# Performance work log

Hardware: AMD Instinct MI355X
Metric: run time of the kernel (lower is better)

## Reference

```python
import jax, jax.numpy as jnp
import numpy as np

V = 10000   # vocab size
H = 768     # HIDDEN_SIZE
B = 8       # batch
S = 512     # padded seq len
L = 8       # TRANSFORMER_LAYERS
EPS = 1e-5  # torch LayerNorm default eps


def setup_inputs() -> dict:
    key = jax.random.key(0)
    ks = jax.random.split(key, 16)
    init = lambda k, shape: jax.random.normal(k, shape, jnp.float32) * 0.02
    x = jax.random.randint(ks[0], (B, S), 0, V)
    # full-length sequences: avoids NaN from the original's softmax(dim=1) over
    # fully -inf padded columns (same behavior as torch for this input)
    lengths = jnp.full((B,), S, dtype=jnp.int32)
    return {
        'x': x,
        'lengths': lengths,
        'emb_w': init(ks[1], (V, H)),
        'Wq': init(ks[2], (L, H, H)), 'bq': jnp.zeros((L, H), jnp.float32),
        'Wk': init(ks[3], (L, H, H)), 'bk': jnp.zeros((L, H), jnp.float32),
        'Wv': init(ks[4], (L, H, H)), 'bv': jnp.zeros((L, H), jnp.float32),
        'W1': init(ks[5], (L, H, H)), 'b1': jnp.zeros((L, H), jnp.float32),
        'W2': init(ks[6], (L, H, H)), 'b2': jnp.zeros((L, H), jnp.float32),
        'g1': jnp.ones((L, H), jnp.float32), 'be1': jnp.zeros((L, H), jnp.float32),
        'g2': jnp.ones((L, H), jnp.float32), 'be2': jnp.zeros((L, H), jnp.float32),
        'fc_w': init(ks[7], (H, H)), 'fc_b': jnp.zeros((H,), jnp.float32),
    }


def _layernorm(x, g, b):
    m = jnp.mean(x, axis=-1, keepdims=True)
    v = jnp.mean(jnp.square(x - m), axis=-1, keepdims=True)
    return (x - m) * jax.lax.rsqrt(v + EPS) * g + b


def _pos_encoding(seq, dim):
    pos = jnp.arange(seq, dtype=jnp.float32)[:, None]
    div = jnp.exp(jnp.arange(0, dim, 2, dtype=jnp.float32) * (-np.log(10000.0) / dim))
    ang = pos * div[None, :]                                  # [S, H/2]
    return jnp.stack([jnp.sin(ang), jnp.cos(ang)], axis=-1).reshape(seq, dim)


def reference(x, lengths, emb_w, Wq, bq, Wk, bk, Wv, bv, W1, b1, W2, b2,
              g1, be1, g2, be2, fc_w, fc_b):
    z = emb_w[x] + _pos_encoding(S, H)[None]                  # [B,S,H]
    causal = jnp.tril(jnp.ones((S, S), bool))                 # [S,S]
    valid = jnp.arange(S)[None, :] < lengths[:, None]         # [B,S]
    mask = causal[None] & valid[:, None, :] & valid[:, :, None]  # [B,S,S]
    scale = 1.0 / jnp.sqrt(jnp.float32(H))
    for i in range(L):
        q = z @ Wq[i] + bq[i]
        k = z @ Wk[i] + bk[i]
        v = z @ Wv[i] + bv[i]
        scores = jnp.einsum('bqh,bkh->bqk', q, k) * scale
        scores = jnp.where(mask, scores, -jnp.inf)
        # NOTE: original code applies softmax over dim=1 (query axis) — faithful
        atten = jax.nn.softmax(scores, axis=1)
        out = jnp.einsum('bqk,bkh->bqh', atten, v)
        o1 = _layernorm(z + out, g1[i], be1[i])               # eval: dropout=identity
        mid = jax.nn.relu(o1 @ W1[i] + b1[i]) @ W2[i] + b2[i]
        z = _layernorm(mid + o1, g2[i], be2[i])
    zf = z @ fc_w + fc_b                                      # [B,S,H]
    logits = jnp.einsum('bsh,vh->bsv', zf, emb_w)             # [B,S,V]
    return jax.nn.softmax(logits, axis=-1)
```

## Files before the change

### kernel.cpp

```cpp
#include <hip/hip_runtime.h>
#include <math.h>

typedef unsigned int   u32;
typedef unsigned short u16;
typedef __attribute__((ext_vector_type(8))) short bf16x8;
typedef __attribute__((ext_vector_type(4))) float f32x4;
typedef __attribute__((ext_vector_type(4))) unsigned short u16x4;
typedef __attribute__((ext_vector_type(8))) unsigned short u16x8;

#define HID   768
#define SEQ   512
#define BATCH 8
#define LAYERS 8
#define VOC   10000
#define NROWS (BATCH*SEQ)
#define NH    ((long long)NROWS*HID)
#define SS8   ((long long)BATCH*SEQ*SEQ)
#define EPSLN 1e-5f
#define WSZ   ((long long)HID*HID)

__device__ __forceinline__ u16 f2bf(float f) {
    u32 u = __builtin_bit_cast(u32, f);
    return (u16)((u + 0x7fffu + ((u >> 16) & 1u)) >> 16);
}
__device__ __forceinline__ float bf2f(u16 h) {
    return __builtin_bit_cast(float, (u32)h << 16);
}

__device__ __forceinline__ void async16(u16* lds, const u16* g) {
    __builtin_amdgcn_global_load_lds(
        (const __attribute__((address_space(1))) u32*)g,
        (__attribute__((address_space(3))) u32*)lds, 16, 0, 0);
}

__global__ __launch_bounds__(256) void embed_kernel(
    const int* __restrict__ x, const float* __restrict__ emb,
    float* __restrict__ Z, u16* __restrict__ Zh)
{
    const int row = blockIdx.x;
    const int s   = row & (SEQ - 1);
    const int tok = x[row];
    const long long base  = (long long)row * HID;
    const long long ebase = (long long)tok * HID;
    const float coef = -0.0239852613853544f;
    #pragma unroll
    for (int j = 0; j < 3; ++j) {
        const int h = threadIdx.x + 256 * j;
        const int i = h >> 1;
        const float ang = (float)s * expf((float)i * coef);
        const float pe  = (h & 1) ? cosf(ang) : sinf(ang);
        const float v = emb[ebase + h] + pe;
        Z[base + h]  = v;
        Zh[base + h] = f2bf(v);
    }
}

__global__ __launch_bounds__(256) void convert_emb(
    const float* __restrict__ e, u16* __restrict__ eh)
{
    const long long i = ((long long)blockIdx.x * 256 + threadIdx.x) * 4;
    const float4 v = *(const float4*)&e[i];
    u16x4 p;
    p[0] = f2bf(v.x); p[1] = f2bf(v.y); p[2] = f2bf(v.z); p[3] = f2bf(v.w);
    *(u16x4*)&eh[i] = p;
}

__global__ __launch_bounds__(256) void transp_all(
    const float* __restrict__ Wq, const float* __restrict__ Wk,
    const float* __restrict__ Wv, const float* __restrict__ W1,
    const float* __restrict__ W2, const float* __restrict__ fcw,
    u16* __restrict__ WT)
{
    __shared__ u16 tile[32][34];
    const int z = blockIdx.z;
    const float* src;
    long long doff;
    if (z < 40) {
        const int lyr = z / 5, idx = z % 5;
        const float* bases[5] = {Wq, Wk, Wv, W1, W2};
        src  = bases[idx] + (long long)lyr * WSZ;
        doff = ((long long)lyr * 5 + idx) * WSZ;
    } else {
        src = fcw; doff = 40LL * WSZ;
    }
    u16* D = WT + doff;
    const int n0 = blockIdx.x * 32, k0 = blockIdx.y * 32;
    const int c = threadIdx.x & 31, r0 = threadIdx.x >> 5;
    #pragma unroll
    for (int p = 0; p < 4; ++p)
        tile[r0 + 8*p][c] = f2bf(src[(long long)(k0 + r0 + 8*p) * HID + n0 + c]);
    __syncthreads();
    #pragma unroll
    for (int p = 0; p < 4; ++p)
        D[(long long)(n0 + r0 + 8*p) * HID + k0 + c] = tile[c][r0 + 8*p];
}

__global__ void pack_bias_all(const float* __restrict__ bq,
                              const float* __restrict__ bk,
                              const float* __restrict__ bv,
                              float* __restrict__ dst)
{
    const int part = blockIdx.x, l = blockIdx.y, h = threadIdx.x;
    const float* src = part == 0 ? bq : (part == 1 ? bk : bv);
    dst[((long long)l*3 + part) * HID + h] = src[(long long)l*HID + h];
}

template<bool RELU, bool OUT_BF16, bool XISM, bool VSPLIT>
__global__ __launch_bounds__(256) void gemm_mfma(
    const u16* __restrict__ A, int lda, long long sA,
    const u16* __restrict__ B, int ldb, long long sB,
    void* __restrict__ Cp, int ldc, long long sC,
    int N, int K, const float* __restrict__ bias, float alpha,
    u16* __restrict__ vt)
{
    __shared__ u16 As[2][128 * 32];
    __shared__ u16 Bs[2][128 * 32];
    const int bz = blockIdx.z;
    const int m0 = (XISM ? blockIdx.x : blockIdx.y) * 128;
    const int n0 = (XISM ? blockIdx.y : blockIdx.x) * 128;
    const int t = threadIdx.x, w = t >> 6, l = t & 63;
    const int lrow = l >> 2, lk8 = (l & 3) * 8;
    const int wm = (w >> 1) * 64, wn = (w & 1) * 64;
    A += sA * bz; B += sB * bz;

    f32x4 acc[4][4];
    #pragma unroll
    for (int mi = 0; mi < 4; ++mi)
        #pragma unroll
        for (int ni = 0; ni < 4; ++ni) acc[mi][ni] = (f32x4){0.f,0.f,0.f,0.f};

    auto stage = [&](int buf, int k0) {
        #pragma unroll
        for (int r = 0; r < 2; ++r) {
            const int seg = w * 2 + r;
            async16(&As[buf][seg * 512],
                    A + (long long)(m0 + seg*16 + lrow) * lda + (k0 + lk8));
        }
        #pragma unroll
        for (int r = 0; r < 2; ++r) {
            const int seg = w * 2 + r;
            int row = n0 + seg*16 + lrow;
            row = row < N ? row : N - 1;
            async16(&Bs[buf][seg * 512], B + (long long)row * ldb + (k0 + lk8));
        }
    };
    const int fr = l & 15, fk = (l >> 4) * 8;
    auto compute = [&](int cur) {
        bf16x8 af[4], bfr[4];
        #pragma unroll
        for (int mi = 0; mi < 4; ++mi)
            af[mi] = *(const bf16x8*)&As[cur][(wm + mi*16 + fr) * 32 + fk];
        #pragma unroll
        for (int ni = 0; ni < 4; ++ni)
            bfr[ni] = *(const bf16x8*)&Bs[cur][(wn + ni*16 + fr) * 32 + fk];
        #pragma unroll
        for (int mi = 0; mi < 4; ++mi)
            #pragma unroll
            for (int ni = 0; ni < 4; ++ni)
                acc[mi][ni] = __builtin_amdgcn_mfma_f32_16x16x32_bf16(
                    af[mi], bfr[ni], acc[mi][ni], 0, 0, 0);
    };

    const int NS = K >> 5;
    stage(0, 0);
    for (int tt = 0; tt < NS; ++tt) {
        if (tt + 1 < NS) {
            stage((tt + 1) & 1, (tt + 1) << 5);
            asm volatile("s_waitcnt vmcnt(4)\n\ts_barrier" ::: "memory");
        } else {
            asm volatile("s_waitcnt vmcnt(0)\n\ts_barrier" ::: "memory");
        }
        compute(tt & 1);
        asm volatile("s_barrier" ::: "memory");
    }

    float* Cf = (float*)Cp + sC * bz;
    u16*   Ch = (u16*)Cp + sC * bz;
    const int fq = l >> 4;
    #pragma unroll
    for (int ni = 0; ni < 4; ++ni) {
        const int col = n0 + wn + ni*16 + fr;
        const bool ok = col < N;
        const float bv = (bias && ok) ? bias[col] : 0.f;
        #pragma unroll
        for (int mi = 0; mi < 4; ++mi) {
            const int row0 = m0 + wm + mi*16 + fq*4;
            if constexpr (VSPLIT) {
                if (col < 1536) {
                    #pragma unroll
                    for (int v = 0; v < 4; ++v)
                        Ch[(long long)(row0 + v) * ldc + col] =
                            f2bf(alpha * acc[mi][ni][v] + bv);
                } else {
                    const int b9 = row0 >> 9, s9 = row0 & 511;
                    u16x4 pk;
                    #pragma unroll
                    for (int v = 0; v < 4; ++v)
                        pk[v] = f2bf(alpha * acc[mi][ni][v] + bv);
                    *(u16x4*)&vt[((long long)b9 * HID + (col - 1536)) * SEQ + s9] = pk;
                }
            } else {
                #pragma unroll
                for (int v = 0; v < 4; ++v) {
                    float val = alpha * acc[mi][ni][v] + bv;
                    if (RELU) val = fmaxf(val, 0.f);
                    if (ok) {
                        if (OUT_BF16) Ch[(long long)(row0 + v) * ldc + col] = f2bf(val);
                        else          Cf[(long long)(row0 + v) * ldc + col] = val;
                    }
                }
            }
        }
    }
}

template<bool RELU, bool OUT_BF16>
__global__ __launch_bounds__(128) void gemm_small(
    const u16* __restrict__ A, int lda, long long sA,
    const u16* __restrict__ B, int ldb, long long sB,
    void* __restrict__ Cp, int ldc, long long sC,
    int N, int K, const float* __restrict__ bias, float alpha)
{
    __shared__ u16 As[2][64 * 64];
    __shared__ u16 Bs[2][64 * 64];
    const int bz = blockIdx.z;
    const int n0 = blockIdx.x * 64;
    const int m0 = blockIdx.y * 64;
    const int t = threadIdx.x, w = t >> 6, l = t & 63;
    const int srow = l >> 3;
    const int skof = ((l & 7) ^ srow) * 8;
    const int wm = w * 32;
    A += sA * bz; B += sB * bz;

    f32x4 acc[2][4];
    #pragma unroll
    for (int mi = 0; mi < 2; ++mi)
        #pragma unroll
        for (int ni = 0; ni < 4; ++ni) acc[mi][ni] = (f32x4){0.f,0.f,0.f,0.f};

    auto stage = [&](int buf, int k0) {
        #pragma unroll
        for (int r = 0; r < 4; ++r) {
            const int seg = w * 4 + r;
            const int row = seg * 8 + srow;
            async16(&As[buf][seg * 512],
                    A + (long long)(m0 + row) * lda + (k0 + skof));
        }
        #pragma unroll
        for (int r = 0; r < 4; ++r) {
            const int seg = w * 4 + r;
            const int row = seg * 8 + srow;
            async16(&Bs[buf][seg * 512],
                    B + (long long)(n0 + row) * ldb + (k0 + skof));
        }
    };
    const int fr = l & 15, fkb = l >> 4;
    auto compute = [&](int cur) {
        #pragma unroll
        for (int ks = 0; ks < 2; ++ks) {
            const int ps = ((ks * 4 + fkb) ^ (fr & 7)) * 8;
            bf16x8 af[2], bfv[4];
            #pragma unroll
            for (int mi = 0; mi < 2; ++mi)
                af[mi] = *(const bf16x8*)&As[cur][(wm + mi*16 + fr) * 64 + ps];
            #pragma unroll
            for (int ni = 0; ni < 4; ++ni)
                bfv[ni] = *(const bf16x8*)&Bs[cur][(ni*16 + fr) * 64 + ps];
            #pragma unroll
            for (int mi = 0; mi < 2; ++mi)
                #pragma unroll
                for (int ni = 0; ni < 4; ++ni)
                    acc[mi][ni] = __builtin_amdgcn_mfma_f32_16x16x32_bf16(
                        af[mi], bfv[ni], acc[mi][ni], 0, 0, 0);
        }
    };

    const int NS = K >> 6;
    stage(0, 0);
    for (int tt = 0; tt < NS; ++tt) {
        if (tt + 1 < NS) {
            stage((tt + 1) & 1, (tt + 1) << 6);
            asm volatile("s_waitcnt vmcnt(8)\n\ts_barrier" ::: "memory");
        } else {
            asm volatile("s_waitcnt vmcnt(0)\n\ts_barrier" ::: "memory");
        }
        compute(tt & 1);
        asm volatile("s_barrier" ::: "memory");
    }

    float* Cf = (float*)Cp + sC * bz;
    u16*   Ch = (u16*)Cp + sC * bz;
    const int fq = l >> 4;
    #pragma unroll
    for (int ni = 0; ni < 4; ++ni) {
        const int col = n0 + ni*16 + fr;
        const float bv = bias ? bias[col] : 0.f;
        #pragma unroll
        for (int mi = 0; mi < 2; ++mi) {
            const int row0 = m0 + wm + mi*16 + fq*4;
            #pragma unroll
            for (int v = 0; v < 4; ++v) {
                float val = alpha * acc[mi][ni][v] + bv;
                if (RELU) val = fmaxf(val, 0.f);
                if (OUT_BF16) Ch[(long long)(row0 + v) * ldc + col] = f2bf(val);
                else          Cf[(long long)(row0 + v) * ldc + col] = val;
            }
        }
    }
}

__global__ __launch_bounds__(256) void gemm_conv(
    const u16* __restrict__ A, const float* __restrict__ Bf,
    u16* __restrict__ C)
{
    __shared__ u16 As[128 * 32];
    __shared__ u16 Bs[128 * 32];
    const int m0 = blockIdx.x * 128;
    const int n0 = blockIdx.y * 128;
    const int t = threadIdx.x, w = t >> 6, l = t & 63;
    const int lrow = l >> 2, lk8 = (l & 3) * 8;
    const int wm = (w >> 1) * 64, wn = (w & 1) * 64;
    f32x4 acc[4][4];
    #pragma unroll
    for (int mi = 0; mi < 4; ++mi)
        #pragma unroll
        for (int ni = 0; ni < 4; ++ni) acc[mi][ni] = (f32x4){0.f,0.f,0.f,0.f};

    for (int k0 = 0; k0 < HID; k0 += 32) {
        #pragma unroll
        for (int r = 0; r < 2; ++r) {
            const int seg = w * 2 + r;
            async16(&As[seg * 512],
                    A + (long long)(m0 + seg*16 + lrow) * HID + (k0 + lk8));
        }
        #pragma unroll
        for (int r = 0; r < 2; ++r) {
            const int flat = r * 2048 + t * 8;
            int row = n0 + (flat >> 5);
            row = row < VOC ? row : VOC - 1;
            const float* g = Bf + (long long)row * HID + (k0 + (flat & 31));
            const float4 v0 = *(const float4*)g;
            const float4 v1 = *(const float4*)(g + 4);
            bf16x8 hv;
            hv[0]=(short)f2bf(v0.x); hv[1]=(short)f2bf(v0.y);
            hv[2]=(short)f2bf(v0.z); hv[3]=(short)f2bf(v0.w);
            hv[4]=(short)f2bf(v1.x); hv[5]=(short)f2bf(v1.y);
            hv[6]=(short)f2bf(v1.z); hv[7]=(short)f2bf(v1.w);
            *(bf16x8*)&Bs[flat] = hv;
        }
        __syncthreads();
        const int fr = l & 15, fk = (l >> 4) * 8;
        bf16x8 af[4], bfr[4];
        #pragma unroll
        for (int mi = 0; mi < 4; ++mi)
            af[mi] = *(const bf16x8*)&As[(wm + mi*16 + fr) * 32 + fk];
        #pragma unroll
        for (int ni = 0; ni < 4; ++ni)
            bfr[ni] = *(const bf16x8*)&Bs[(wn + ni*16 + fr) * 32 + fk];
        #pragma unroll
        for (int mi = 0; mi < 4; ++mi)
            #pragma unroll
            for (int ni = 0; ni < 4; ++ni)
                acc[mi][ni] = __builtin_amdgcn_mfma_f32_16x16x32_bf16(
                    af[mi], bfr[ni], acc[mi][ni], 0, 0, 0);
        __syncthreads();
    }
    const int fr = l & 15, fq = l >> 4;
    #pragma unroll
    for (int ni = 0; ni < 4; ++ni) {
        const int col = n0 + wn + ni*16 + fr;
        if (col >= VOC) continue;
        #pragma unroll
        for (int mi = 0; mi < 4; ++mi) {
            const int row0 = m0 + wm + mi*16 + fq*4;
            #pragma unroll
            for (int v = 0; v < 4; ++v)
                C[(long long)(row0 + v) * (2*VOC) + col] = f2bf(acc[mi][ni][v]);
        }
    }
}

__global__ __launch_bounds__(256) void softmax_q_kernel(
    const float* __restrict__ sc, u16* __restrict__ att,
    const int* __restrict__ lengths)
{
    const int b  = blockIdx.x;
    const int k0 = blockIdx.y * 16;
    const int tx = threadIdx.x & 15;
    const int ty = threadIdx.x >> 4;
    const int c  = k0 + tx;
    const int len = lengths[b];
    const float* base  = sc  + (long long)b * SEQ * SEQ;
    u16*         obase = att + (long long)b * SEQ * SEQ;
    const bool cvalid = (c < len);

    float vals[32];
    float m = -3.0e38f, ssum = 0.f;
    #pragma unroll
    for (int i = 0; i < 32; ++i) {
        const int q = ty + 16 * i;
        float xv = -3.0e38f;
        if (cvalid && c <= q && q < len)
            xv = base[(long long)q * SEQ + c];
        vals[i] = xv;
        if (xv > m) { ssum = ssum * __expf(m - xv) + 1.f; m = xv; }
        else if (xv > -3.0e38f) { ssum += __expf(xv - m); }
    }
    __shared__ float ms[16][17], ss[16][17];
    ms[ty][tx] = m; ss[ty][tx] = ssum;
    __syncthreads();
    if (ty == 0) {
        float M = ms[0][tx];
        #pragma unroll
        for (int r = 1; r < 16; ++r) M = fmaxf(M, ms[r][tx]);
        float Sx = 0.f;
        #pragma unroll
        for (int r = 0; r < 16; ++r) Sx += ss[r][tx] * __expf(ms[r][tx] - M);
        ms[0][tx] = M; ss[0][tx] = Sx;
    }
    __syncthreads();
    const float M   = ms[0][tx];
    const float den = ss[0][tx];
    const float inv = (den > 0.f) ? 1.f / den : 0.f;
    #pragma unroll
    for (int i = 0; i < 32; ++i) {
        const int q = ty + 16 * i;
        obase[(long long)q * SEQ + c] = f2bf(__expf(vals[i] - M) * inv);
    }
}

__global__ __launch_bounds__(256) void ln_add_kernel(
    const float* __restrict__ Xa, const float* __restrict__ Xb,
    float* __restrict__ O, u16* __restrict__ Oh,
    const float* __restrict__ g, const float* __restrict__ be)
{
    const int row = blockIdx.x;
    const long long base = (long long)row * HID;
    const int t = threadIdx.x;
    const float x0 = Xa[base + t]       + Xb[base + t];
    const float x1 = Xa[base + t + 256] + Xb[base + t + 256];
    const float x2 = Xa[base + t + 512] + Xb[base + t + 512];
    __shared__ float r1[4], r2[4];
    float s = x0 + x1 + x2;
    #pragma unroll
    for (int o = 32; o; o >>= 1) s += __shfl_down(s, o, 64);
    if ((t & 63) == 0) r1[t >> 6] = s;
    __syncthreads();
    const float mean = (r1[0] + r1[1] + r1[2] + r1[3]) * (1.f / HID);
    const float d0 = x0 - mean, d1 = x1 - mean, d2 = x2 - mean;
    float v = d0*d0 + d1*d1 + d2*d2;
    #pragma unroll
    for (int o = 32; o; o >>= 1) v += __shfl_down(v, o, 64);
    if ((t & 63) == 0) r2[t >> 6] = v;
    __syncthreads();
    const float var = (r2[0] + r2[1] + r2[2] + r2[3]) * (1.f / HID);
    const float rs = rsqrtf(var + EPSLN);
    const float y0 = d0 * rs * g[t]       + be[t];
    const float y1 = d1 * rs * g[t + 256] + be[t + 256];
    const float y2 = d2 * rs * g[t + 512] + be[t + 512];
    O[base + t]        = y0;  Oh[base + t]       = f2bf(y0);
    O[base + t + 256]  = y1;  Oh[base + t + 256] = f2bf(y1);
    O[base + t + 512]  = y2;  Oh[base + t + 512] = f2bf(y2);
}

__global__ __launch_bounds__(256) void softmax_v_kernel(float* __restrict__ out)
{
    __shared__ float row[VOC];
    __shared__ float rm[4], rs_[4];
    const long long obase = (long long)blockIdx.x * VOC;
    const u16* lg = (const u16*)out + 2 * obase + VOC;
    const int t = threadIdx.x;
    float m = -3.0e38f, s = 0.f;
    for (int i = t * 8; i < VOC; i += 2048) {
        const u16x8 h8 = *(const u16x8*)&lg[i];
        #pragma unroll
        for (int j = 0; j < 8; ++j) {
            const float xv = bf2f(h8[j]);
            row[i + j] = xv;
            const float d = xv - m;
            if (d > 0.f) { s = s * __expf(-d) + 1.f; m = xv; }
            else         { s += __expf(d); }
        }
    }
    #pragma unroll
    for (int o = 32; o; o >>= 1) {
        const float om = __shfl_down(m, o, 64), os = __shfl_down(s, o, 64);
        const float M = fmaxf(m, om);
        s = s * __expf(m - M) + os * __expf(om - M);
        m = M;
    }
    if ((t & 63) == 0) { rm[t >> 6] = m; rs_[t >> 6] = s; }
    __syncthreads();
    const float M = fmaxf(fmaxf(rm[0], rm[1]), fmaxf(rm[2], rm[3]));
    const float S = rs_[0]*__expf(rm[0]-M) + rs_[1]*__expf(rm[1]-M)
                  + rs_[2]*__expf(rm[2]-M) + rs_[3]*__expf(rm[3]-M);
    const float inv = 1.f / S;
    for (int i = t * 4; i < VOC; i += 1024) {
        float4 v = *(const float4*)&row[i];
        v.x = __expf(v.x - M) * inv;
        v.y = __expf(v.y - M) * inv;
        v.z = __expf(v.z - M) * inv;
        v.w = __expf(v.w - M) * inv;
        *(float4*)&out[obase + i] = v;
    }
}

extern "C" void kernel_launch(void* const* d_in, const int* in_sizes, int n_in,
                              void* d_out, int out_size, void* d_ws, size_t ws_size,
                              hipStream_t stream)
{
    const int*   x    = (const int*)  d_in[0];
    const int*   lens = (const int*)  d_in[1];
    const float* emb  = (const float*)d_in[2];
    const float* Wq   = (const float*)d_in[3];
    const float* bq   = (const float*)d_in[4];
    const float* Wk   = (const float*)d_in[5];
    const float* bk   = (const float*)d_in[6];
    const float* Wv   = (const float*)d_in[7];
    const float* bv   = (const float*)d_in[8];
    const float* W1   = (const float*)d_in[9];
    const float* b1   = (const float*)d_in[10];
    const float* W2   = (const float*)d_in[11];
    const float* b2   = (const float*)d_in[12];
    const float* g1   = (const float*)d_in[13];
    const float* be1  = (const float*)d_in[14];
    const float* g2   = (const float*)d_in[15];
    const float* be2  = (const float*)d_in[16];
    const float* fcw  = (const float*)d_in[17];
    const float* fcb  = (const float*)d_in[18];

    float* out = (float*)d_out;
    float* Zb     = out;
    float* O1f    = Zb + NH;
    float* M2f    = O1f + NH;
    float* SCORES = M2f + NH;
    float* BQKV   = SCORES + SS8;
    u16* ub   = (u16*)(BQKV + (long long)LAYERS * 2304);
    u16* Zbh  = ub;  ub += NH;
    u16* QKVh = ub;  ub += (long long)NROWS * 1536;
    u16* ATTB = ub;  ub += SS8;
    u16* Vt   = ub;  ub += NH;
    u16* O1h  = ub;  ub += NH;
    u16* M1h  = ub;  ub += NH;
    u16* WT   = ub;  ub += 41LL * WSZ;

    u16* ZFh = (u16*)d_ws;
    u16* EH  = ZFh + NH;
    const bool ehpath = ws_size >= (size_t)((NH + (long long)VOC * HID) * 2);
    u16* LOGH = (u16*)out + VOC;

    const float scale = 1.0f / sqrtf((float)HID);
    const dim3 blk(256), blk128(128);

    embed_kernel<<<NROWS, blk, 0, stream>>>(x, emb, Zb, Zbh);
    transp_all<<<dim3(24, 24, 41), blk, 0, stream>>>(Wq, Wk, Wv, W1, W2, fcw, WT);
    pack_bias_all<<<dim3(3, LAYERS), dim3(768), 0, stream>>>(bq, bk, bv, BQKV);
    if (ehpath) convert_emb<<<7500, blk, 0, stream>>>(emb, EH);

    for (int l = 0; l < LAYERS; ++l) {
        const u16* wl = WT + (long long)l * 5 * WSZ;

        gemm_mfma<false, true, false, true><<<dim3(18, 32), blk, 0, stream>>>(
            Zbh, HID, 0, wl, HID, 0, QKVh, 1536, 0,
            2304, HID, BQKV + (long long)l * 2304, 1.0f, Vt);

        gemm_small<false, false><<<dim3(8, 8, BATCH), blk128, 0, stream>>>(
            QKVh, 1536, (long long)SEQ * 1536,
            QKVh + 768, 1536, (long long)SEQ * 1536,
            SCORES, SEQ, (long long)SEQ * SEQ,
            512, HID, nullptr, scale);

        softmax_q_kernel<<<dim3(BATCH, SEQ/16), blk, 0, stream>>>(SCORES, ATTB, lens);

        gemm_small<false, false><<<dim3(12, 8, BATCH), blk128, 0, stream>>>(
            ATTB, SEQ, (long long)SEQ * SEQ,
            Vt, SEQ, (long long)HID * SEQ,
            O1f, HID, (long long)SEQ * HID,
            768, SEQ, nullptr, 1.0f);

        ln_add_kernel<<<NROWS, blk, 0, stream>>>(Zb, O1f, O1f, O1h,
                                                 g1 + l*HID, be1 + l*HID);
        gemm_small<true, true><<<dim3(12, 64), blk128, 0, stream>>>(
            O1h, HID, 0, wl + 3*WSZ, HID, 0, M1h, HID, 0,
            768, HID, b1 + l*HID, 1.0f);
        gemm_small<false, false><<<dim3(12, 64), blk128, 0, stream>>>(
            M1h, HID, 0, wl + 4*WSZ, HID, 0, M2f, HID, 0,
            768, HID, b2 + l*HID, 1.0f);
        ln_add_kernel<<<NROWS, blk, 0, stream>>>(M2f, O1f, Zb, Zbh,
                                                 g2 + l*HID, be2 + l*HID);
    }

    gemm_small<false, true><<<dim3(12, 64), blk128, 0, stream>>>(
        Zbh, HID, 0, WT + 40LL*WSZ, HID, 0, ZFh, HID, 0,
        768, HID, fcb, 1.0f);

    if (ehpath) {
        gemm_mfma<false, true, true, false><<<dim3(32, 79), blk, 0, stream>>>(
            ZFh, HID, 0, EH, HID, 0, LOGH, 2*VOC, 0,
            VOC, HID, nullptr, 1.0f, nullptr);
    } else {
        gemm_conv<<<dim3(32, 79), blk, 0, stream>>>(ZFh, emb, LOGH);
    }

    softmax_v_kernel<<<NROWS, blk, 0, stream>>>(out);
}
```

Measured before the change: 1.095 ms.

## Replace 128x128 MFMA GEMM with 256x256 swizzled 8-wave kernel; warp-per-row LayerNorm

The 128x128 MFMA GEMM used for the QKV projection and the vocab logits is replaced by a 512-thread kernel with 256x256 tiles, K-steps of 64 split into two halves, and an XOR-swizzled LDS layout. Global loads are interleaved between MFMA groups, with s_setprio raising wave priority around the matrix math. The intent is more reuse per tile, fewer LDS bank conflicts and better overlap of loads with compute. LayerNorm now handles one row per wavefront with float4 loads and shuffle-only reductions, removing shared-memory barriers. The larger tiles mean fewer blocks (144 for QKV) on a 256-CU part and higher register pressure, which may hurt occupancy.

```diff
diff --git a/kernel.cpp b/kernel.cpp
--- a/kernel.cpp
+++ b/kernel.cpp
@@ -105,110 +105,125 @@
     dst[((long long)l*3 + part) * HID + h] = src[(long long)l*HID + h];
 }
 
-template<bool RELU, bool OUT_BF16, bool XISM, bool VSPLIT>
-__global__ __launch_bounds__(256) void gemm_mfma(
-    const u16* __restrict__ A, int lda, long long sA,
-    const u16* __restrict__ B, int ldb, long long sB,
-    void* __restrict__ Cp, int ldc, long long sC,
-    int N, int K, const float* __restrict__ bias, float alpha,
-    u16* __restrict__ vt)
-{
-    __shared__ u16 As[2][128 * 32];
-    __shared__ u16 Bs[2][128 * 32];
-    const int bz = blockIdx.z;
-    const int m0 = (XISM ? blockIdx.x : blockIdx.y) * 128;
-    const int n0 = (XISM ? blockIdx.y : blockIdx.x) * 128;
+template<bool VSPLIT>
+__global__ __launch_bounds__(512) void gemm_8ph(
+    const u16* __restrict__ A, const u16* __restrict__ B,
+    u16* __restrict__ Cp, int ldc, int N, int K,
+    const float* __restrict__ bias, u16* __restrict__ vt)
+{
+    __shared__ u16 Ab[2][2][8192];
+    __shared__ u16 Bb[2][2][8192];
+    const int m0 = blockIdx.x * 256;
+    const int n0 = blockIdx.y * 256;
     const int t = threadIdx.x, w = t >> 6, l = t & 63;
-    const int lrow = l >> 2, lk8 = (l & 3) * 8;
-    const int wm = (w >> 1) * 64, wn = (w & 1) * 64;
-    A += sA * bz; B += sB * bz;
-
-    f32x4 acc[4][4];
-    #pragma unroll
-    for (int mi = 0; mi < 4; ++mi)
-        #pragma unroll
-        for (int ni = 0; ni < 4; ++ni) acc[mi][ni] = (f32x4){0.f,0.f,0.f,0.f};
-
-    auto stage = [&](int buf, int k0) {
+    const int fr = l & 15, jl = l >> 4;
+    const int wm = (w >> 2) * 128, wn = (w & 3) * 64;
+
+    f32x4 acc[8][4];
+    #pragma unroll
+    for (int mf = 0; mf < 8; ++mf)
+        #pragma unroll
+        for (int nf = 0; nf < 4; ++nf) acc[mf][nf] = (f32x4){0.f,0.f,0.f,0.f};
+
+    auto stageA = [&](int d, int h, int kt) {
         #pragma unroll
         for (int r = 0; r < 2; ++r) {
-            const int seg = w * 2 + r;
-            async16(&As[buf][seg * 512],
-                    A + (long long)(m0 + seg*16 + lrow) * lda + (k0 + lk8));
-        }
+            const int f16 = r * 512 + t;
+            const int row = f16 >> 2, j = f16 & 3;
+            const int kofs = kt + h * 32 + ((j ^ ((row >> 1) & 3)) << 3);
+            async16(&Ab[d][h][f16 * 8], A + (long long)(m0 + row) * K + kofs);
+        }
+    };
+    auto stageB = [&](int d, int h, int kt) {
         #pragma unroll
         for (int r = 0; r < 2; ++r) {
-            const int seg = w * 2 + r;
-            int row = n0 + seg*16 + lrow;
-            row = row < N ? row : N - 1;
-            async16(&Bs[buf][seg * 512], B + (long long)row * ldb + (k0 + lk8));
+            const int f16 = r * 512 + t;
+            const int row = f16 >> 2, j = f16 & 3;
+            int gr = n0 + row; gr = gr < N ? gr : N - 1;
+            const int kofs = kt + h * 32 + ((j ^ ((row >> 1) & 3)) << 3);
+            async16(&Bb[d][h][f16 * 8], B + (long long)gr * K + kofs);
         }
     };
-    const int fr = l & 15, fk = (l >> 4) * 8;
-    auto compute = [&](int cur) {
-        bf16x8 af[4], bfr[4];
-        #pragma unroll
-        for (int mi = 0; mi < 4; ++mi)
-            af[mi] = *(const bf16x8*)&As[cur][(wm + mi*16 + fr) * 32 + fk];
-        #pragma unroll
-        for (int ni = 0; ni < 4; ++ni)
-            bfr[ni] = *(const bf16x8*)&Bs[cur][(wn + ni*16 + fr) * 32 + fk];
-        #pragma unroll
-        for (int mi = 0; mi < 4; ++mi)
-            #pragma unroll
-            for (int ni = 0; ni < 4; ++ni)
-                acc[mi][ni] = __builtin_amdgcn_mfma_f32_16x16x32_bf16(
-                    af[mi], bfr[ni], acc[mi][ni], 0, 0, 0);
-    };
-
-    const int NS = K >> 5;
-    stage(0, 0);
-    for (int tt = 0; tt < NS; ++tt) {
-        if (tt + 1 < NS) {
-            stage((tt + 1) & 1, (tt + 1) << 5);
-            asm volatile("s_waitcnt vmcnt(4)\n\ts_barrier" ::: "memory");
-        } else {
-            asm volatile("s_waitcnt vmcnt(0)\n\ts_barrier" ::: "memory");
-        }
-        compute(tt & 1);
-        asm volatile("s_barrier" ::: "memory");
-    }
-
-    float* Cf = (float*)Cp + sC * bz;
-    u16*   Ch = (u16*)Cp + sC * bz;
-    const int fq = l >> 4;
-    #pragma unroll
-    for (int ni = 0; ni < 4; ++ni) {
-        const int col = n0 + wn + ni*16 + fr;
-        const bool ok = col < N;
-        const float bv = (bias && ok) ? bias[col] : 0.f;
-        #pragma unroll
-        for (int mi = 0; mi < 4; ++mi) {
-            const int row0 = m0 + wm + mi*16 + fq*4;
+
+    stageA(0, 0, 0); stageB(0, 0, 0); stageA(0, 1, 0); stageB(0, 1, 0);
+
+    const int NT = K >> 6;
+    for (int tt = 0; tt < NT; ++tt) {
+        const int d = tt & 1, kt1 = (tt + 1) << 6;
+        const bool more = (tt + 1) < NT;
+        #pragma unroll
+        for (int h = 0; h < 2; ++h) {
+            if (h == 0 || more) asm volatile("s_waitcnt vmcnt(4)" ::: "memory");
+            else                asm volatile("s_waitcnt vmcnt(0)" ::: "memory");
+            __builtin_amdgcn_s_barrier();
+            asm volatile("" ::: "memory");
+            if (more) stageA(d ^ 1, h, kt1);
+            bf16x8 bfr[4], af[4];
+            #pragma unroll
+            for (int nf = 0; nf < 4; ++nf) {
+                const int row = wn + nf * 16 + fr;
+                bfr[nf] = *(const bf16x8*)
+                    &Bb[d][h][row * 32 + ((jl ^ ((row >> 1) & 3)) << 3)];
+            }
+            #pragma unroll
+            for (int mi = 0; mi < 4; ++mi) {
+                const int row = wm + mi * 16 + fr;
+                af[mi] = *(const bf16x8*)
+                    &Ab[d][h][row * 32 + ((jl ^ ((row >> 1) & 3)) << 3)];
+            }
+            __builtin_amdgcn_s_setprio(1);
+            #pragma unroll
+            for (int mi = 0; mi < 4; ++mi)
+                #pragma unroll
+                for (int nf = 0; nf < 4; ++nf)
+                    acc[mi][nf] = __builtin_amdgcn_mfma_f32_16x16x32_bf16(
+                        af[mi], bfr[nf], acc[mi][nf], 0, 0, 0);
+            __builtin_amdgcn_s_setprio(0);
+            if (more) stageB(d ^ 1, h, kt1);
+            #pragma unroll
+            for (int mi = 0; mi < 4; ++mi) {
+                const int row = wm + (mi + 4) * 16 + fr;
+                af[mi] = *(const bf16x8*)
+                    &Ab[d][h][row * 32 + ((jl ^ ((row >> 1) & 3)) << 3)];
+            }
+            __builtin_amdgcn_s_setprio(1);
+            #pragma unroll
+            for (int mi = 0; mi < 4; ++mi)
+                #pragma unroll
+                for (int nf = 0; nf < 4; ++nf)
+                    acc[mi + 4][nf] = __builtin_amdgcn_mfma_f32_16x16x32_bf16(
+                        af[mi], bfr[nf], acc[mi + 4][nf], 0, 0, 0);
+            __builtin_amdgcn_s_setprio(0);
+        }
+    }
+
+    #pragma unroll
+    for (int nf = 0; nf < 4; ++nf) {
+        const int col = n0 + wn + nf * 16 + fr;
+        if (col >= N) continue;
+        const float bv = bias ? bias[col] : 0.f;
+        #pragma unroll
+        for (int mf = 0; mf < 8; ++mf) {
+            const int row0 = m0 + wm + mf * 16 + jl * 4;
             if constexpr (VSPLIT) {
                 if (col < 1536) {
                     #pragma unroll
                     for (int v = 0; v < 4; ++v)
-                        Ch[(long long)(row0 + v) * ldc + col] =
-                            f2bf(alpha * acc[mi][ni][v] + bv);
+                        Cp[(long long)(row0 + v) * ldc + col] =
+                            f2bf(acc[mf][nf][v] + bv);
                 } else {
                     const int b9 = row0 >> 9, s9 = row0 & 511;
                     u16x4 pk;
                     #pragma unroll
                     for (int v = 0; v < 4; ++v)
-                        pk[v] = f2bf(alpha * acc[mi][ni][v] + bv);
+                        pk[v] = f2bf(acc[mf][nf][v] + bv);
                     *(u16x4*)&vt[((long long)b9 * HID + (col - 1536)) * SEQ + s9] = pk;
                 }
             } else {
                 #pragma unroll
-                for (int v = 0; v < 4; ++v) {
-                    float val = alpha * acc[mi][ni][v] + bv;
-                    if (RELU) val = fmaxf(val, 0.f);
-                    if (ok) {
-                        if (OUT_BF16) Ch[(long long)(row0 + v) * ldc + col] = f2bf(val);
-                        else          Cf[(long long)(row0 + v) * ldc + col] = val;
-                    }
-                }
+                for (int v = 0; v < 4; ++v)
+                    Cp[(long long)(row0 + v) * ldc + col] =
+                        f2bf(acc[mf][nf][v] + bv);
             }
         }
     }
@@ -434,33 +449,45 @@
     float* __restrict__ O, u16* __restrict__ Oh,
     const float* __restrict__ g, const float* __restrict__ be)
 {
-    const int row = blockIdx.x;
+    const int row = blockIdx.x * 4 + (threadIdx.x >> 6);
+    const int l = threadIdx.x & 63;
     const long long base = (long long)row * HID;
-    const int t = threadIdx.x;
-    const float x0 = Xa[base + t]       + Xb[base + t];
-    const float x1 = Xa[base + t + 256] + Xb[base + t + 256];
-    const float x2 = Xa[base + t + 512] + Xb[base + t + 512];
-    __shared__ float r1[4], r2[4];
-    float s = x0 + x1 + x2;
-    #pragma unroll
-    for (int o = 32; o; o >>= 1) s += __shfl_down(s, o, 64);
-    if ((t & 63) == 0) r1[t >> 6] = s;
-    __syncthreads();
-    const float mean = (r1[0] + r1[1] + r1[2] + r1[3]) * (1.f / HID);
-    const float d0 = x0 - mean, d1 = x1 - mean, d2 = x2 - mean;
-    float v = d0*d0 + d1*d1 + d2*d2;
-    #pragma unroll
-    for (int o = 32; o; o >>= 1) v += __shfl_down(v, o, 64);
-    if ((t & 63) == 0) r2[t >> 6] = v;
-    __syncthreads();
-    const float var = (r2[0] + r2[1] + r2[2] + r2[3]) * (1.f / HID);
-    const float rs = rsqrtf(var + EPSLN);
-    const float y0 = d0 * rs * g[t]       + be[t];
-    const float y1 = d1 * rs * g[t + 256] + be[t + 256];
-    const float y2 = d2 * rs * g[t + 512] + be[t + 512];
-    O[base + t]        = y0;  Oh[base + t]       = f2bf(y0);
-    O[base + t + 256]  = y1;  Oh[base + t + 256] = f2bf(y1);
-    O[base + t + 512]  = y2;  Oh[base + t + 512] = f2bf(y2);
+    float x[12];
+    #pragma unroll
+    for (int c = 0; c < 3; ++c) {
+        const int off = c * 256 + l * 4;
+        const float4 a = *(const float4*)&Xa[base + off];
+        const float4 b = *(const float4*)&Xb[base + off];
+        x[c*4+0] = a.x + b.x; x[c*4+1] = a.y + b.y;
+        x[c*4+2] = a.z + b.z; x[c*4+3] = a.w + b.w;
+    }
+    float s = 0.f;
+    #pragma unroll
+    for (int i = 0; i < 12; ++i) s += x[i];
+    #pragma unroll
+    for (int o = 32; o; o >>= 1) s += __shfl_xor(s, o, 64);
+    const float mean = s * (1.f / HID);
+    float v = 0.f;
+    #pragma unroll
+    for (int i = 0; i < 12; ++i) { const float d = x[i] - mean; v += d * d; }
+    #pragma unroll
+    for (int o = 32; o; o >>= 1) v += __shfl_xor(v, o, 64);
+    const float rs = rsqrtf(v * (1.f / HID) + EPSLN);
+    #pragma unroll
+    for (int c = 0; c < 3; ++c) {
+        const int off = c * 256 + l * 4;
+        const float4 gg = *(const float4*)&g[off];
+        const float4 bb = *(const float4*)&be[off];
+        float4 y;
+        y.x = (x[c*4+0] - mean) * rs * gg.x + bb.x;
+        y.y = (x[c*4+1] - mean) * rs * gg.y + bb.y;
+        y.z = (x[c*4+2] - mean) * rs * gg.z + bb.z;
+        y.w = (x[c*4+3] - mean) * rs * gg.w + bb.w;
+        *(float4*)&O[base + off] = y;
+        u16x4 p;
+        p[0] = f2bf(y.x); p[1] = f2bf(y.y); p[2] = f2bf(y.z); p[3] = f2bf(y.w);
+        *(u16x4*)&Oh[base + off] = p;
+    }
 }
 
 __global__ __launch_bounds__(256) void softmax_v_kernel(float* __restrict__ out)
@@ -550,7 +577,7 @@
     u16* LOGH = (u16*)out + VOC;
 
     const float scale = 1.0f / sqrtf((float)HID);
-    const dim3 blk(256), blk128(128);
+    const dim3 blk(256), blk128(128), blk512(512);
 
     embed_kernel<<<NROWS, blk, 0, stream>>>(x, emb, Zb, Zbh);
     transp_all<<<dim3(24, 24, 41), blk, 0, stream>>>(Wq, Wk, Wv, W1, W2, fcw, WT);
@@ -560,9 +587,9 @@
     for (int l = 0; l < LAYERS; ++l) {
         const u16* wl = WT + (long long)l * 5 * WSZ;
 
-        gemm_mfma<false, true, false, true><<<dim3(18, 32), blk, 0, stream>>>(
-            Zbh, HID, 0, wl, HID, 0, QKVh, 1536, 0,
-            2304, HID, BQKV + (long long)l * 2304, 1.0f, Vt);
+        gemm_8ph<true><<<dim3(16, 9), blk512, 0, stream>>>(
+            Zbh, wl, QKVh, 1536, 2304, HID,
+            BQKV + (long long)l * 2304, Vt);
 
         gemm_small<false, false><<<dim3(8, 8, BATCH), blk128, 0, stream>>>(
             QKVh, 1536, (long long)SEQ * 1536,
@@ -578,16 +605,16 @@
             O1f, HID, (long long)SEQ * HID,
             768, SEQ, nullptr, 1.0f);
 
-        ln_add_kernel<<<NROWS, blk, 0, stream>>>(Zb, O1f, O1f, O1h,
-                                                 g1 + l*HID, be1 + l*HID);
+        ln_add_kernel<<<NROWS/4, blk, 0, stream>>>(Zb, O1f, O1f, O1h,
+                                                   g1 + l*HID, be1 + l*HID);
         gemm_small<true, true><<<dim3(12, 64), blk128, 0, stream>>>(
             O1h, HID, 0, wl + 3*WSZ, HID, 0, M1h, HID, 0,
             768, HID, b1 + l*HID, 1.0f);
         gemm_small<false, false><<<dim3(12, 64), blk128, 0, stream>>>(
             M1h, HID, 0, wl + 4*WSZ, HID, 0, M2f, HID, 0,
             768, HID, b2 + l*HID, 1.0f);
-        ln_add_kernel<<<NROWS, blk, 0, stream>>>(M2f, O1f, Zb, Zbh,
-                                                 g2 + l*HID, be2 + l*HID);
+        ln_add_kernel<<<NROWS/4, blk, 0, stream>>>(M2f, O1f, Zb, Zbh,
+                                                   g2 + l*HID, be2 + l*HID);
     }
 
     gemm_small<false, true><<<dim3(12, 64), blk128, 0, stream>>>(
@@ -595,9 +622,8 @@
         768, HID, fcb, 1.0f);
 
     if (ehpath) {
-        gemm_mfma<false, true, true, false><<<dim3(32, 79), blk, 0, stream>>>(
-            ZFh, HID, 0, EH, HID, 0, LOGH, 2*VOC, 0,
-            VOC, HID, nullptr, 1.0f, nullptr);
+        gemm_8ph<false><<<dim3(16, 40), blk512, 0, stream>>>(
+            ZFh, EH, LOGH, 2*VOC, VOC, HID, nullptr, nullptr);
     } else {
         gemm_conv<<<dim3(32, 79), blk, 0, stream>>>(ZFh, emb, LOGH);
     }
```

Result: slower. 1.143 ms (+4.3%).
